# Kernel optimization log

Hardware: AMD Instinct MI355X
Metric: run time of the kernel (lower is better)

The kernel has to match this reference:

```python
import jax, jax.numpy as jnp
import numpy as np

B, C, H, W, E, HEADS = 8, 128, 96, 96, 16, 4
HD = C // HEADS

def _ln(x, g, b, eps=1e-5):
    m = jnp.mean(x, axis=-1, keepdims=True)
    v = jnp.mean(jnp.square(x - m), axis=-1, keepdims=True)
    return (x - m) * jax.lax.rsqrt(v + eps) * g + b

def _gelu(x):
    return jax.nn.gelu(x, approximate=False)  # torch nn.GELU default (erf)

def setup_inputs() -> dict:
    key = jax.random.key(0)
    ks = iter(jax.random.split(key, 48))
    def wgt(shape, s=0.02):
        return jax.random.normal(next(ks), shape, jnp.float32) * s
    d = {
        "feature_map": jax.random.normal(next(ks), (B, C, H, W), jnp.float32),
        "hyperedge_scores": jax.random.uniform(next(ks), (B, H * W, E), jnp.float32),
        # norm_node_pre
        "np_g": jnp.ones((C,), jnp.float32), "np_b": jnp.zeros((C,), jnp.float32),
        # MultiheadAttention (self-attn over hyperedges)
        "mha_w_in": wgt((3 * C, C)), "mha_b_in": jnp.zeros((3 * C,), jnp.float32),
        "mha_w_out": wgt((C, C)), "mha_b_out": jnp.zeros((C,), jnp.float32),
        # transformer FFN
        "ffn_w1": wgt((2 * C, C)), "ffn_b1": jnp.zeros((2 * C,), jnp.float32),
        "ffn_w2": wgt((C, 2 * C)), "ffn_b2": jnp.zeros((C,), jnp.float32),
        # shared LayerNorm inside HypergraphTransformerConv (used twice)
        "tnorm_g": jnp.ones((C,), jnp.float32), "tnorm_b": jnp.zeros((C,), jnp.float32),
        # norm_hyper
        "nh_g": jnp.ones((C,), jnp.float32), "nh_b": jnp.zeros((C,), jnp.float32),
        # hyper_proj
        "hp_w": wgt((C, C)), "hp_b": jnp.zeros((C,), jnp.float32),
        # HyperedgeGuidedNodeAttention
        "q_w": wgt((C, C)), "q_b": jnp.zeros((C,), jnp.float32),
        "kv_w": wgt((2 * C, C)), "kv_b": jnp.zeros((2 * C,), jnp.float32),
        # norm_fusion
        "nf_g": jnp.ones((2 * C,), jnp.float32), "nf_b": jnp.zeros((2 * C,), jnp.float32),
        # gate = Linear(2C->C) + LayerNorm(C) + Sigmoid
        "gate_w": wgt((C, 2 * C)), "gate_b": jnp.zeros((C,), jnp.float32),
        "gate_ln_g": jnp.ones((C,), jnp.float32), "gate_ln_b": jnp.zeros((C,), jnp.float32),
        # node_proj
        "nproj_w": wgt((C, C)), "nproj_b": jnp.zeros((C,), jnp.float32),
    }
    return d

def _forward(feature_map, hyperedge_scores, np_g, np_b, mha_w_in, mha_b_in,
             mha_w_out, mha_b_out, ffn_w1, ffn_b1, ffn_w2, ffn_b2,
             tnorm_g, tnorm_b, nh_g, nh_b, hp_w, hp_b, q_w, q_b, kv_w, kv_b,
             nf_g, nf_b, gate_w, gate_b, gate_ln_g, gate_ln_b, nproj_w, nproj_b):
    b, c, h, w = feature_map.shape
    n = h * w
    node = jnp.transpose(feature_map.reshape(b, c, n), (0, 2, 1))   # [B,N,C]
    node = _ln(node, np_g, np_b)
    # hyperedge aggregation: H^T @ X -> [B,E,C]
    hyper = jnp.einsum('bne,bnc->bec', hyperedge_scores, node)
    # --- HypergraphTransformerConv (self-attn over E=16 hyperedges) ---
    qkv = hyper @ mha_w_in.T + mha_b_in                               # [B,E,3C]
    q, k, v = jnp.split(qkv, 3, axis=-1)
    def heads(x):  # [B,E,C] -> [B,h,E,hd]
        return jnp.transpose(x.reshape(b, E, HEADS, HD), (0, 2, 1, 3))
    q, k, v = heads(q), heads(k), heads(v)
    attn = jax.nn.softmax(jnp.einsum('bhqd,bhkd->bhqk', q, k) / np.sqrt(HD), axis=-1)
    ao = jnp.einsum('bhqk,bhkd->bhqd', attn, v)
    ao = jnp.transpose(ao, (0, 2, 1, 3)).reshape(b, E, c)
    ao = ao @ mha_w_out.T + mha_b_out
    x = _ln(hyper + ao, tnorm_g, tnorm_b)
    ffn = _gelu(x @ ffn_w1.T + ffn_b1) @ ffn_w2.T + ffn_b2
    hyper = _ln(x + ffn, tnorm_g, tnorm_b)
    # ---
    hyper = _ln(hyper, nh_g, nh_b)
    hyper = _gelu(hyper @ hp_w.T + hp_b)                              # [B,E,C]
    intra = jnp.einsum('bne,bec->bnc', hyperedge_scores, hyper)       # [B,N,C]
    # HyperedgeGuidedNodeAttention (scale = C**-0.5)
    Q = node @ q_w.T + q_b
    K, V = jnp.split(hyper @ kv_w.T + kv_b, 2, axis=-1)
    a = jax.nn.softmax(jnp.einsum('bnc,bec->bne', Q, K) * (c ** -0.5), axis=-1)
    cross = jnp.einsum('bne,bec->bnc', a, V)
    combined = _ln(jnp.concatenate([intra, cross], axis=-1), nf_g, nf_b)
    gate = jax.nn.sigmoid(_ln(combined @ gate_w.T + gate_b, gate_ln_g, gate_ln_b))
    fused = gate * intra + (1.0 - gate) * cross
    upd = node + fused                                                # dropout in eval mode
    out = _gelu(upd @ nproj_w.T + nproj_b)
    return jnp.transpose(out, (0, 2, 1)).reshape(b, c, h, w)

def reference(feature_map, hyperedge_scores, np_g, np_b, mha_w_in, mha_b_in,
              mha_w_out, mha_b_out, ffn_w1, ffn_b1, ffn_w2, ffn_b2,
              tnorm_g, tnorm_b, nh_g, nh_b, hp_w, hp_b, q_w, q_b, kv_w, kv_b,
              nf_g, nf_b, gate_w, gate_b, gate_ln_g, gate_ln_b, nproj_w, nproj_b):
    return _forward(feature_map, hyperedge_scores, np_g, np_b, mha_w_in, mha_b_in,
                    mha_w_out, mha_b_out, ffn_w1, ffn_b1, ffn_w2, ffn_b2,
                    tnorm_g, tnorm_b, nh_g, nh_b, hp_w, hp_b, q_w, q_b, kv_w, kv_b,
                    nf_g, nf_b, gate_w, gate_b, gate_ln_g, gate_ln_b, nproj_w, nproj_b)
```

## Files before the change

### kernel.cpp

```cpp
#include <hip/hip_runtime.h>

typedef unsigned short bf_t;
typedef unsigned int u32;
typedef short short8 __attribute__((ext_vector_type(8)));
typedef float f32x4 __attribute__((ext_vector_type(4)));

#define NB 8
#define CC 128
#define NN 9216
#define EE 16

__device__ __forceinline__ float b2f(bf_t u){ return __uint_as_float(((u32)u)<<16); }
__device__ __forceinline__ bf_t f2b(float f){
  u32 u = __float_as_uint(f);
  u = (u + 0x7fffu + ((u>>16)&1u)) >> 16;
  return (bf_t)u;
}
__device__ __forceinline__ float gelu_f(float x){ return 0.5f*x*(1.f+erff(x*0.70710678118654752f)); }
__device__ __forceinline__ float red16(float v){
  #pragma unroll
  for (int m=1;m<16;m<<=1) v += __shfl_xor(v, m, 16);
  return v;
}
__device__ __forceinline__ float grs(float var){
  return rsqrtf(fmaxf(var + 1e-5f, 1e-8f));
}
__device__ __forceinline__ short8 ldw8(const float* __restrict__ p){
  float4 a = *(const float4*)p;
  float4 b = *(const float4*)(p+4);
  short8 o;
  o[0]=(short)f2b(a.x); o[1]=(short)f2b(a.y); o[2]=(short)f2b(a.z); o[3]=(short)f2b(a.w);
  o[4]=(short)f2b(b.x); o[5]=(short)f2b(b.y); o[6]=(short)f2b(b.z); o[7]=(short)f2b(b.w);
  return o;
}

template<int MODE>
__global__ __launch_bounds__(256) void k_pre(float* __restrict__ hacc,
    const float* __restrict__ gw, const float* __restrict__ npw,
    bf_t* __restrict__ gwb, bf_t* __restrict__ npwb,
    const float* __restrict__ w_in, const float* __restrict__ w_out,
    const float* __restrict__ w1, const float* __restrict__ w2,
    const float* __restrict__ hpw, const float* __restrict__ kvw,
    const float* __restrict__ qw,
    bf_t* __restrict__ w_in_b, bf_t* __restrict__ w_out_b,
    bf_t* __restrict__ w1_b, bf_t* __restrict__ w2_b,
    bf_t* __restrict__ hpw_b, bf_t* __restrict__ kvw_b,
    bf_t* __restrict__ qwT_b){
  int i = blockIdx.x*256 + threadIdx.x;
  hacc[i] = 0.f;
  if (MODE >= 1){
    gwb[i]       = f2b(gw[i]);
    gwb[i+16384] = f2b(gw[i+16384]);
    npwb[i]      = f2b(npw[i]);
  }
  if (MODE == 2){
    #pragma unroll
    for (int k=0;k<3;k++) w_in_b[i + k*16384] = f2b(w_in[i + k*16384]);
    w_out_b[i]       = f2b(w_out[i]);
    w1_b[i]          = f2b(w1[i]);
    w1_b[i+16384]    = f2b(w1[i+16384]);
    w2_b[i]          = f2b(w2[i]);
    w2_b[i+16384]    = f2b(w2[i+16384]);
    hpw_b[i]         = f2b(hpw[i]);
    kvw_b[i]         = f2b(kvw[i]);
    kvw_b[i+16384]   = f2b(kvw[i+16384]);
    qwT_b[i]         = f2b(qw[(i&127)*128 + (i>>7)]);
  }
}

template<int BFOUT>
__global__ __launch_bounds__(256,4) void k_ln_agg(const float* __restrict__ fm,
                                                  const float* __restrict__ g,
                                                  const float* __restrict__ bb,
                                                  const float* __restrict__ sc,
                                                  float* __restrict__ nln,
                                                  bf_t* __restrict__ nlnb,
                                                  float* __restrict__ hacc){
  int b = blockIdx.y, n0 = blockIdx.x*64, tid = threadIdx.x;
  __shared__ float xs[128*65];
  __shared__ float scs[64][17];
  __shared__ float ps[4][64], pq[4][64], mrs[2][64];
  const float* base = fm + (size_t)b*CC*NN + n0;
  #pragma unroll
  for (int p=0;p<8;p++){
    int idx = tid + p*256;
    int c = idx>>4, n4 = (idx&15)*4;
    float4 v = *(const float4*)(base + (size_t)c*NN + n4);
    xs[c*65 + n4+0] = v.x; xs[c*65 + n4+1] = v.y;
    xs[c*65 + n4+2] = v.z; xs[c*65 + n4+3] = v.w;
  }
  { int n = tid>>2, e4 = (tid&3)*4;
    float4 sv = *(const float4*)(sc + ((size_t)(b*NN + n0 + n))*EE + e4);
    scs[n][e4+0] = sv.x; scs[n][e4+1] = sv.y;
    scs[n][e4+2] = sv.z; scs[n][e4+3] = sv.w;
  }
  __syncthreads();
  { int cg = tid>>6, n = tid&63;
    float s=0.f, q=0.f;
    #pragma unroll
    for (int c=0;c<32;c++){ float v = xs[(cg*32+c)*65 + n]; s+=v; q+=v*v; }
    ps[cg][n]=s; pq[cg][n]=q;
  }
  __syncthreads();
  if (tid < 64){
    float S = ps[0][tid]+ps[1][tid]+ps[2][tid]+ps[3][tid];
    float Q = pq[0][tid]+pq[1][tid]+pq[2][tid]+pq[3][tid];
    float m = S*(1.f/128.f);
    mrs[0][tid] = m; mrs[1][tid] = grs(Q*(1.f/128.f) - m*m);
  }
  __syncthreads();
  #pragma unroll
  for (int p=0;p<8;p++){
    int idx = tid + p*256;
    int c = idx>>4, n4 = (idx&15)*4;
    float gv = g[c], bv = bb[c];
    float v0 = (xs[c*65+n4+0]-mrs[0][n4+0])*mrs[1][n4+0]*gv + bv;
    float v1 = (xs[c*65+n4+1]-mrs[0][n4+1])*mrs[1][n4+1]*gv + bv;
    float v2 = (xs[c*65+n4+2]-mrs[0][n4+2])*mrs[1][n4+2]*gv + bv;
    float v3 = (xs[c*65+n4+3]-mrs[0][n4+3])*mrs[1][n4+3]*gv + bv;
    xs[c*65+n4+0]=v0; xs[c*65+n4+1]=v1; xs[c*65+n4+2]=v2; xs[c*65+n4+3]=v3;
    if (!BFOUT){
      float4 o; o.x=v0; o.y=v1; o.z=v2; o.w=v3;
      *(float4*)(nln + ((size_t)(b*CC + c))*NN + n0 + n4) = o;
    }
  }
  __syncthreads();
  if (BFOUT){
    #pragma unroll
    for (int p=0;p<4;p++){
      int idx = tid + p*256;
      int n = idx>>4, c8 = (idx&15)*8;
      short8 o;
      #pragma unroll
      for (int j=0;j<8;j++) o[j] = (short)f2b(xs[(c8+j)*65 + n]);
      *(short8*)(nlnb + ((size_t)(b*NN + n0 + n))*CC + c8) = o;
    }
  }
  { int cp = tid&63, eh = tid>>6;
    float a0[4]={0,0,0,0}, a1[4]={0,0,0,0};
    for (int n=0;n<64;n++){
      float x0 = xs[cp*65 + n], x1 = xs[(cp+64)*65 + n];
      #pragma unroll
      for (int j=0;j<4;j++){
        float se = scs[n][eh*4+j];
        a0[j] += se*x0; a1[j] += se*x1;
      }
    }
    #pragma unroll
    for (int j=0;j<4;j++){
      float* hb = hacc + (size_t)(b*EE + eh*4 + j)*CC;
      atomicAdd(hb + cp, a0[j]);
      atomicAdd(hb + cp + 64, a1[j]);
    }
  }
}

template<int K, int NOUT, int ACT, int WB>
__device__ __forceinline__ void gemm16(const bf_t* A, int SA,
                                       const float* __restrict__ W,
                                       const bf_t* __restrict__ Wb,
                                       const float* __restrict__ bias,
                                       bf_t* O, int SO, int tid){
  int lane = tid&63, wid = tid>>6;
  int m16 = lane&15, quad = lane>>4;
  #pragma unroll
  for (int u=0; u<NOUT/64; u++){
    int n0 = u*64 + wid*16;
    f32x4 acc = {0.f,0.f,0.f,0.f};
    #pragma unroll
    for (int k0=0;k0<K;k0+=32){
      short8 af = *(const short8*)(A + m16*SA + k0 + quad*8);
      short8 bfv = WB ? *(const short8*)(Wb + (size_t)(n0+m16)*K + k0 + quad*8)
                      : ldw8(W + (size_t)(n0+m16)*K + k0 + quad*8);
      acc = __builtin_amdgcn_mfma_f32_16x16x32_bf16(af, bfv, acc, 0, 0, 0);
    }
    int col = n0 + m16;
    float bv = bias[col];
    #pragma unroll
    for (int r=0;r<4;r++){
      float v = acc[r] + bv;
      if (ACT) v = gelu_f(v);
      O[(quad*4+r)*SO + col] = f2b(v);
    }
  }
}

#define SP1 136
#define SP2 264
#define SP3 392

template<int WB>
__global__ __launch_bounds__(256) void k_edge(const float* __restrict__ hacc,
    const float* w_in, const float* b_in, const float* w_out, const float* b_out,
    const float* w1, const float* b1, const float* w2, const float* b2v,
    const float* tg, const float* tb, const float* nhg, const float* nhb,
    const float* hpw, const float* hpb, const float* kvw, const float* kvbias,
    const float* qw, const float* qb,
    const bf_t* __restrict__ w_in_b, const bf_t* __restrict__ w_out_b,
    const bf_t* __restrict__ w1_b, const bf_t* __restrict__ w2_b,
    const bf_t* __restrict__ hpw_b, const bf_t* __restrict__ kvw_b,
    const bf_t* __restrict__ qwT_b,
    bf_t* __restrict__ hfw, bf_t* __restrict__ vws,
    bf_t* __restrict__ Ktgb, float* __restrict__ qbK){
  __shared__ __align__(16) bf_t hyp0[16*SP1];
  __shared__ __align__(16) bf_t qkvb[16*SP3];
  __shared__ __align__(16) bf_t aob [16*SP1];
  __shared__ __align__(16) bf_t xnb [16*SP1];
  __shared__ __align__(16) bf_t h1b [16*SP2];
  __shared__ __align__(16) bf_t t2b [16*SP1];
  __shared__ __align__(16) bf_t hfb [16*SP1];
  __shared__ __align__(16) bf_t kvo [16*SP2];
  int b = blockIdx.x, tid = threadIdx.x;
  int lane = tid&63, wid = tid>>6, m16 = lane&15, quad = lane>>4;

  #pragma unroll
  for (int p=0;p<8;p++){
    int idx = tid + p*256;
    int e = idx>>7, c = idx&127;
    hyp0[e*SP1 + c] = f2b(hacc[(size_t)(b*EE + e)*CC + c]);
  }
  __syncthreads();
  gemm16<128,384,0,WB>(hyp0, SP1, w_in, w_in_b, b_in, qkvb, SP3, tid);
  __syncthreads();
  {
    int part = tid&3, hq = tid>>2;
    int h = hq>>4, qi = hq&15;
    int dbase = h*32 + part*8;
    float qv[8];
    #pragma unroll
    for (int j=0;j<8;j++) qv[j] = b2f(qkvb[qi*SP3 + dbase + j]);
    float dot[16];
    #pragma unroll
    for (int kk=0;kk<16;kk++){
      float s = 0.f;
      #pragma unroll
      for (int j=0;j<8;j++) s += qv[j]*b2f(qkvb[kk*SP3 + 128 + dbase + j]);
      dot[kk] = s;
    }
    #pragma unroll
    for (int m=1;m<4;m<<=1){
      #pragma unroll
      for (int kk=0;kk<16;kk++) dot[kk] += __shfl_xor(dot[kk], m, 4);
    }
    const float sc1 = 0.17677669529663687f;
    float mx = -1e30f;
    #pragma unroll
    for (int kk=0;kk<16;kk++){ dot[kk] *= sc1; mx = fmaxf(mx, dot[kk]); }
    float sum = 0.f;
    #pragma unroll
    for (int kk=0;kk<16;kk++){ dot[kk] = __expf(dot[kk]-mx); sum += dot[kk]; }
    float inv = 1.f/sum;
    float ao[8] = {0,0,0,0,0,0,0,0};
    #pragma unroll
    for (int kk=0;kk<16;kk++){
      float p = dot[kk]*inv;
      #pragma unroll
      for (int j=0;j<8;j++) ao[j] += p*b2f(qkvb[kk*SP3 + 256 + dbase + j]);
    }
    #pragma unroll
    for (int j=0;j<8;j++) aob[qi*SP1 + dbase + j] = f2b(ao[j]);
  }
  __syncthreads();
  gemm16<128,128,0,WB>(aob, SP1, w_out, w_out_b, b_out, xnb, SP1, tid);
  __syncthreads();
  {
    int e = tid>>4, i = tid&15;
    float v[8]; float s=0.f, q=0.f;
    #pragma unroll
    for (int j=0;j<8;j++){
      int c = i*8+j;
      v[j] = b2f(hyp0[e*SP1+c]) + b2f(xnb[e*SP1+c]);
      s += v[j]; q += v[j]*v[j];
    }
    s = red16(s); q = red16(q);
    float m = s*(1.f/128.f);
    float rs = grs(q*(1.f/128.f) - m*m);
    #pragma unroll
    for (int j=0;j<8;j++){
      int c = i*8+j;
      xnb[e*SP1+c] = f2b((v[j]-m)*rs*tg[c] + tb[c]);
    }
  }
  __syncthreads();
  gemm16<128,256,1,WB>(xnb, SP1, w1, w1_b, b1, h1b, SP2, tid);
  __syncthreads();
  gemm16<256,128,0,WB>(h1b, SP2, w2, w2_b, b2v, aob, SP1, tid);
  __syncthreads();
  {
    int e = tid>>4, i = tid&15;
    float v[8]; float s=0.f, q=0.f;
    #pragma unroll
    for (int j=0;j<8;j++){
      int c = i*8+j;
      v[j] = b2f(xnb[e*SP1+c]) + b2f(aob[e*SP1+c]);
      s += v[j]; q += v[j]*v[j];
    }
    s = red16(s); q = red16(q);
    float m = s*(1.f/128.f);
    float rs = grs(q*(1.f/128.f) - m*m);
    float s2=0.f, q2=0.f;
    #pragma unroll
    for (int j=0;j<8;j++){
      int c = i*8+j;
      v[j] = (v[j]-m)*rs*tg[c] + tb[c];
      s2 += v[j]; q2 += v[j]*v[j];
    }
    s2 = red16(s2); q2 = red16(q2);
    float m2 = s2*(1.f/128.f);
    float rs2 = grs(q2*(1.f/128.f) - m2*m2);
    #pragma unroll
    for (int j=0;j<8;j++){
      int c = i*8+j;
      t2b[e*SP1+c] = f2b((v[j]-m2)*rs2*nhg[c] + nhb[c]);
    }
  }
  __syncthreads();
  gemm16<128,128,1,WB>(t2b, SP1, hpw, hpw_b, hpb, hfb, SP1, tid);
  __syncthreads();
  gemm16<128,256,0,WB>(hfb, SP1, kvw, kvw_b, kvbias, kvo, SP2, tid);
  __syncthreads();
  #pragma unroll
  for (int p=0;p<8;p++){
    int idx = tid + p*256;
    int e = idx>>7, c = idx&127;
    size_t o = (size_t)(b*EE + e)*CC + c;
    hfw[o] = hfb[e*SP1 + c];
    vws[o] = kvo[e*SP2 + 128 + c];
  }
  #pragma unroll
  for (int u=0;u<2;u++){
    int n0 = u*64 + wid*16;
    f32x4 acc = {0.f,0.f,0.f,0.f};
    #pragma unroll
    for (int k0=0;k0<128;k0+=32){
      short8 a = *(const short8*)(kvo + m16*SP2 + k0 + quad*8);
      short8 bq;
      if (WB){
        bq = *(const short8*)(qwT_b + (size_t)(n0+m16)*128 + k0 + quad*8);
      } else {
        #pragma unroll
        for (int j=0;j<8;j++)
          bq[j] = (short)f2b(qw[(size_t)(k0+quad*8+j)*128 + n0+m16]);
      }
      acc = __builtin_amdgcn_mfma_f32_16x16x32_bf16(a, bq, acc, 0, 0, 0);
    }
    #pragma unroll
    for (int r=0;r<4;r++)
      Ktgb[(size_t)(b*EE + quad*4 + r)*CC + n0 + m16] = f2b(acc[r]);
  }
  { int e = tid>>4, i = tid&15;
    float s = 0.f;
    #pragma unroll
    for (int j=0;j<8;j++) s += qb[i*8+j]*b2f(kvo[e*SP2 + i*8+j]);
    s = red16(s);
    if (i == 0) qbK[b*EE + e] = s;
  }
}

template<int MODE>
__global__ __launch_bounds__(256,3) void k_meganode(
    float* __restrict__ io, const bf_t* __restrict__ nlnb,
    const float* __restrict__ sc,
    const bf_t* __restrict__ hf, const bf_t* __restrict__ vw,
    const bf_t* __restrict__ ktg, const float* __restrict__ qbK,
    const float* __restrict__ nfg, const float* __restrict__ nfb,
    const float* __restrict__ gw, const bf_t* __restrict__ gwb,
    const float* __restrict__ gb,
    const float* __restrict__ glng, const float* __restrict__ glnb,
    const float* __restrict__ npw, const bf_t* __restrict__ npwb,
    const float* __restrict__ npb){
  int tid = threadIdx.x, lane = tid&63, wid = tid>>6;
  int m16 = lane&15, quad = lane>>4;
  int b = blockIdx.y, n0 = blockIdx.x*64;
  __shared__ __align__(16) char sm[34816];
  bf_t* xt  = (bf_t*)(sm);
  bf_t* ktT = (bf_t*)(sm + 17408);
  bf_t* hfT = (bf_t*)(sm + 21760);
  bf_t* vfT = (bf_t*)(sm + 25856);
  bf_t* ash = (bf_t*)(sm + 29952);
  bf_t* ct  = (bf_t*)(sm + 17408);
  float* ot = (float*)(sm);
  const short8 z8 = {0,0,0,0,0,0,0,0};

  if (MODE == 2){
    const bf_t* nb = nlnb + ((size_t)(b*NN + n0))*CC;
    #pragma unroll
    for (int p=0;p<4;p++){
      int idx = tid + p*256;
      int n = idx>>4, c8 = (idx&15)*8;
      *(short8*)&xt[n*136 + c8] = *(const short8*)(nb + (size_t)n*CC + c8);
    }
  } else {
    #pragma unroll
    for (int p=0;p<8;p++){
      int idx = tid + p*256;
      int c = idx>>4, n4 = (idx&15)*4;
      float4 v = *(const float4*)(io + ((size_t)(b*CC + c))*NN + n0 + n4);
      xt[(n4+0)*136 + c] = f2b(v.x);
      xt[(n4+1)*136 + c] = f2b(v.y);
      xt[(n4+2)*136 + c] = f2b(v.z);
      xt[(n4+3)*136 + c] = f2b(v.w);
    }
  }
  { const u32* kp = (const u32*)(ktg + (size_t)b*EE*CC);
    #pragma unroll
    for (int p=0;p<4;p++){
      int idx = tid + p*256;
      int e = idx>>6, c2 = (idx&63)*2;
      *(u32*)&ktT[e*136 + c2] = kp[idx];
    }
  }
  { const u32* hs = (const u32*)(hf + (size_t)b*EE*CC);
    const u32* vs = (const u32*)(vw + (size_t)b*EE*CC);
    #pragma unroll
    for (int p=0;p<4;p++){
      int idx = tid + p*256;
      int e = idx>>6, c2 = (idx&63)*2;
      u32 hv = hs[idx], vv = vs[idx];
      hfT[(c2+0)*16 + e] = (bf_t)(hv&0xffffu);
      hfT[(c2+1)*16 + e] = (bf_t)(hv>>16);
      vfT[(c2+0)*16 + e] = (bf_t)(vv&0xffffu);
      vfT[(c2+1)*16 + e] = (bf_t)(vv>>16);
    }
  }
  __syncthreads();

  f32x4 dacc = {0.f,0.f,0.f,0.f};
  #pragma unroll
  for (int kk=0;kk<4;kk++){
    short8 a = *(const short8*)(xt + (wid*16+m16)*136 + kk*32 + quad*8);
    short8 bfr = *(const short8*)(ktT + m16*136 + kk*32 + quad*8);
    dacc = __builtin_amdgcn_mfma_f32_16x16x32_bf16(a, bfr, dacc, 0, 0, 0);
  }
  { float qbe = qbK[b*EE + m16];
    #pragma unroll
    for (int r=0;r<4;r++){
      float v = (dacc[r] + qbe) * 0.08838834764831845f;
      float m = v;
      #pragma unroll
      for (int msk=1;msk<16;msk<<=1) m = fmaxf(m, __shfl_xor(m, msk, 16));
      float ex = __expf(v - m);
      float s = ex;
      #pragma unroll
      for (int msk=1;msk<16;msk<<=1) s += __shfl_xor(s, msk, 16);
      ash[(wid*16 + quad*4 + r)*16 + m16] = f2b(ex / s);
    }
  }

  short8 scf = z8, asf = z8;
  if (quad < 2){
    const float* sp = sc + ((size_t)(b*NN + n0 + wid*16 + m16))*EE + quad*8;
    float4 u0 = *(const float4*)sp;
    float4 u1 = *(const float4*)(sp+4);
    scf[0]=(short)f2b(u0.x); scf[1]=(short)f2b(u0.y); scf[2]=(short)f2b(u0.z); scf[3]=(short)f2b(u0.w);
    scf[4]=(short)f2b(u1.x); scf[5]=(short)f2b(u1.y); scf[6]=(short)f2b(u1.z); scf[7]=(short)f2b(u1.w);
    asf = *(const short8*)(ash + (wid*16+m16)*16 + quad*8);
  }
  f32x4 acc_it[8], acc_cr[8];
  #pragma unroll
  for (int t=0;t<8;t++){
    short8 bh = z8, bv = z8;
    if (quad < 2){
      bh = *(const short8*)(hfT + (t*16+m16)*16 + quad*8);
      bv = *(const short8*)(vfT + (t*16+m16)*16 + quad*8);
    }
    f32x4 zf = {0.f,0.f,0.f,0.f};
    acc_it[t] = __builtin_amdgcn_mfma_f32_16x16x32_bf16(scf, bh, zf, 0, 0, 0);
    acc_cr[t] = __builtin_amdgcn_mfma_f32_16x16x32_bf16(asf, bv, zf, 0, 0, 0);
  }

  float mean4[4], rstd4[4];
  { float s4[4]={0,0,0,0}, q4[4]={0,0,0,0};
    #pragma unroll
    for (int t=0;t<8;t++)
      #pragma unroll
      for (int r=0;r<4;r++){
        float a = acc_it[t][r], c = acc_cr[t][r];
        s4[r] += a + c; q4[r] += a*a + c*c;
      }
    #pragma unroll
    for (int r=0;r<4;r++){
      s4[r] = red16(s4[r]); q4[r] = red16(q4[r]);
      mean4[r] = s4[r]*(1.f/256.f);
      rstd4[r] = grs(q4[r]*(1.f/256.f) - mean4[r]*mean4[r]);
    }
  }
  __syncthreads();
  short8 af[8];
  #pragma unroll
  for (int r=0;r<4;r++){
    int node = wid*16 + quad*4 + r;
    #pragma unroll
    for (int t=0;t<8;t++){
      int ch = t*16 + m16;
      ct[node*136 + ch] = f2b((acc_it[t][r]-mean4[r])*rstd4[r]*nfg[ch] + nfb[ch]);
    }
  }
  #pragma unroll
  for (int kk=0;kk<4;kk++)
    af[kk] = *(const short8*)(ct + (wid*16+m16)*136 + kk*32 + quad*8);
  #pragma unroll
  for (int r=0;r<4;r++){
    int node = wid*16 + quad*4 + r;
    #pragma unroll
    for (int t=0;t<8;t++){
      int ch = t*16 + m16;
      ct[node*136 + ch] = f2b((acc_cr[t][r]-mean4[r])*rstd4[r]*nfg[128+ch] + nfb[128+ch]);
    }
  }
  #pragma unroll
  for (int kk=0;kk<4;kk++)
    af[4+kk] = *(const short8*)(ct + (wid*16+m16)*136 + kk*32 + quad*8);

  f32x4 acc_g[8];
  #pragma unroll
  for (int t=0;t<8;t++){
    f32x4 a = {0.f,0.f,0.f,0.f};
    #pragma unroll
    for (int kk=0;kk<8;kk++){
      short8 w8 = (MODE >= 1) ? *(const short8*)(gwb + (size_t)(t*16+m16)*256 + kk*32 + quad*8)
                              : ldw8(gw + (size_t)(t*16+m16)*256 + kk*32 + quad*8);
      a = __builtin_amdgcn_mfma_f32_16x16x32_bf16(af[kk], w8, a, 0, 0, 0);
    }
    acc_g[t] = a;
  }

  { float s2[4]={0,0,0,0}, q2[4]={0,0,0,0};
    #pragma unroll
    for (int t=0;t<8;t++){
      float bv = gb[t*16+m16];
      #pragma unroll
      for (int r=0;r<4;r++){
        float v = acc_g[t][r] + bv;
        acc_g[t][r] = v; s2[r] += v; q2[r] += v*v;
      }
    }
    #pragma unroll
    for (int r=0;r<4;r++){ s2[r] = red16(s2[r]); q2[r] = red16(q2[r]); }
    #pragma unroll
    for (int t=0;t<8;t++){
      int col = t*16 + m16;
      float lg = glng[col], lb = glnb[col];
      #pragma unroll
      for (int r=0;r<4;r++){
        float m2 = s2[r]*(1.f/128.f);
        float rs2 = grs(q2[r]*(1.f/128.f) - m2*m2);
        float z = (acc_g[t][r]-m2)*rs2*lg + lb;
        float gs = 1.f/(1.f + __expf(-z));
        int node = wid*16 + quad*4 + r;
        float nld = b2f(xt[node*136 + col]);
        xt[node*136 + col] = f2b(nld + gs*acc_it[t][r] + (1.f-gs)*acc_cr[t][r]);
      }
    }
  }

  short8 bfu[4];
  #pragma unroll
  for (int kk=0;kk<4;kk++)
    bfu[kk] = *(const short8*)(xt + (wid*16+m16)*136 + kk*32 + quad*8);
  __syncthreads();
  #pragma unroll
  for (int mt=0;mt<8;mt++){
    f32x4 o = {0.f,0.f,0.f,0.f};
    #pragma unroll
    for (int kk=0;kk<4;kk++){
      short8 aw = (MODE >= 1) ? *(const short8*)(npwb + (size_t)(mt*16+m16)*128 + kk*32 + quad*8)
                              : ldw8(npw + (size_t)(mt*16+m16)*128 + kk*32 + quad*8);
      o = __builtin_amdgcn_mfma_f32_16x16x32_bf16(aw, bfu[kk], o, 0, 0, 0);
    }
    #pragma unroll
    for (int r=0;r<4;r++){
      int cp = mt*16 + quad*4 + r;
      ot[cp*68 + wid*16 + m16] = gelu_f(o[r] + npb[cp]);
    }
  }
  __syncthreads();
  #pragma unroll
  for (int p=0;p<8;p++){
    int idx = tid + p*256;
    int c = idx>>4, n4 = (idx&15)*4;
    float4 v = *(const float4*)&ot[c*68 + n4];
    *(float4*)(io + ((size_t)(b*CC + c))*NN + n0 + n4) = v;
  }
}

extern "C" void kernel_launch(void* const* d_in, const int* in_sizes, int n_in,
                              void* d_out, int out_size, void* d_ws, size_t ws_size,
                              hipStream_t stream){
  (void)in_sizes; (void)n_in; (void)out_size;
  const float* fm   = (const float*)d_in[0];
  const float* sc   = (const float*)d_in[1];
  const float* npg  = (const float*)d_in[2];
  const float* npb_ = (const float*)d_in[3];
  const float* w_in = (const float*)d_in[4];
  const float* b_in = (const float*)d_in[5];
  const float* w_out= (const float*)d_in[6];
  const float* b_out= (const float*)d_in[7];
  const float* w1   = (const float*)d_in[8];
  const float* b1   = (const float*)d_in[9];
  const float* w2   = (const float*)d_in[10];
  const float* b2v  = (const float*)d_in[11];
  const float* tg   = (const float*)d_in[12];
  const float* tb   = (const float*)d_in[13];
  const float* nhg  = (const float*)d_in[14];
  const float* nhb  = (const float*)d_in[15];
  const float* hpw  = (const float*)d_in[16];
  const float* hpb  = (const float*)d_in[17];
  const float* qw   = (const float*)d_in[18];
  const float* qb   = (const float*)d_in[19];
  const float* kvw  = (const float*)d_in[20];
  const float* kvb  = (const float*)d_in[21];
  const float* nfg  = (const float*)d_in[22];
  const float* nfb  = (const float*)d_in[23];
  const float* gw   = (const float*)d_in[24];
  const float* gb   = (const float*)d_in[25];
  const float* glng = (const float*)d_in[26];
  const float* glnb = (const float*)d_in[27];
  const float* npw  = (const float*)d_in[28];
  const float* npb2 = (const float*)d_in[29];

  float* nln = (float*)d_out;

  char* w = (char*)d_ws;
  float* hacc    = (float*)(w);
  float* qbK     = (float*)(w + 65536);
  bf_t*  hfw     = (bf_t*) (w + 66048);
  bf_t*  vws     = (bf_t*) (w + 98816);
  bf_t*  Ktgb    = (bf_t*) (w + 131584);
  bf_t*  gwb     = (bf_t*) (w + 164352);
  bf_t*  npwb    = (bf_t*) (w + 229888);
  bf_t*  w_in_b  = (bf_t*) (w + 262656);
  bf_t*  w_out_b = (bf_t*) (w + 360960);
  bf_t*  w1_b    = (bf_t*) (w + 393728);
  bf_t*  w2_b    = (bf_t*) (w + 459264);
  bf_t*  hpw_b   = (bf_t*) (w + 524800);
  bf_t*  kvw_b   = (bf_t*) (w + 557568);
  bf_t*  qwT_b   = (bf_t*) (w + 623104);
  bf_t*  nlnb    = (bf_t*) (w + 655872);
  bool full = (ws_size >= (size_t)19530240);
  bool pre  = (ws_size >= (size_t)262656);

  if (full){
    k_pre<2><<<dim3(64), dim3(256), 0, stream>>>(hacc, gw, npw, gwb, npwb,
        w_in, w_out, w1, w2, hpw, kvw, qw,
        w_in_b, w_out_b, w1_b, w2_b, hpw_b, kvw_b, qwT_b);
    k_ln_agg<1><<<dim3(144,8), dim3(256), 0, stream>>>(fm, npg, npb_, sc, nln, nlnb, hacc);
    k_edge<1><<<dim3(8), dim3(256), 0, stream>>>(hacc, w_in,b_in,w_out,b_out,
        w1,b1,w2,b2v, tg,tb, nhg,nhb, hpw,hpb, kvw,kvb, qw,qb,
        w_in_b, w_out_b, w1_b, w2_b, hpw_b, kvw_b, qwT_b,
        hfw, vws, Ktgb, qbK);
    k_meganode<2><<<dim3(144,8), dim3(256), 0, stream>>>(nln, nlnb, sc, hfw, vws, Ktgb, qbK,
        nfg, nfb, gw, gwb, gb, glng, glnb, npw, npwb, npb2);
  } else if (pre){
    k_pre<1><<<dim3(64), dim3(256), 0, stream>>>(hacc, gw, npw, gwb, npwb,
        w_in, w_out, w1, w2, hpw, kvw, qw,
        w_in_b, w_out_b, w1_b, w2_b, hpw_b, kvw_b, qwT_b);
    k_ln_agg<0><<<dim3(144,8), dim3(256), 0, stream>>>(fm, npg, npb_, sc, nln, nlnb, hacc);
    k_edge<0><<<dim3(8), dim3(256), 0, stream>>>(hacc, w_in,b_in,w_out,b_out,
        w1,b1,w2,b2v, tg,tb, nhg,nhb, hpw,hpb, kvw,kvb, qw,qb,
        w_in_b, w_out_b, w1_b, w2_b, hpw_b, kvw_b, qwT_b,
        hfw, vws, Ktgb, qbK);
    k_meganode<1><<<dim3(144,8), dim3(256), 0, stream>>>(nln, nlnb, sc, hfw, vws, Ktgb, qbK,
        nfg, nfb, gw, gwb, gb, glng, glnb, npw, npwb, npb2);
  } else {
    k_pre<0><<<dim3(64), dim3(256), 0, stream>>>(hacc, gw, npw, gwb, npwb,
        w_in, w_out, w1, w2, hpw, kvw, qw,
        w_in_b, w_out_b, w1_b, w2_b, hpw_b, kvw_b, qwT_b);
    k_ln_agg<0><<<dim3(144,8), dim3(256), 0, stream>>>(fm, npg, npb_, sc, nln, nlnb, hacc);
    k_edge<0><<<dim3(8), dim3(256), 0, stream>>>(hacc, w_in,b_in,w_out,b_out,
        w1,b1,w2,b2v, tg,tb, nhg,nhb, hpw,hpb, kvw,kvb, qw,qb,
        w_in_b, w_out_b, w1_b, w2_b, hpw_b, kvw_b, qwT_b,
        hfw, vws, Ktgb, qbK);
    k_meganode<0><<<dim3(144,8), dim3(256), 0, stream>>>(nln, nlnb, sc, hfw, vws, Ktgb, qbK,
        nfg, nfb, gw, gwb, gb, glng, glnb, npw, npwb, npb2);
  }
}
```

Measured before the change: 267.9 us.

## Replace hyperedge atomics with partial-sum buffer plus reduction, widen edge kernel to 512 threads

The per-tile hyperedge aggregation now writes per-block partial sums to a workspace buffer, and a new small reduction kernel sums them, replacing global float atomics. The aim is to remove atomic contention on a small accumulator and make the result deterministic. The edge kernel goes from 256 to 512 threads, with the MFMA GEMMs split across 8 waves, to shorten its serial chain of small GEMMs. The cost is an extra launch and about 9 MB of partial-sum traffic. The new path runs only when the workspace is large enough.

```diff
diff --git a/kernel.cpp b/kernel.cpp
--- a/kernel.cpp
+++ b/kernel.cpp
@@ -9,6 +9,7 @@
 #define CC 128
 #define NN 9216
 #define EE 16
+#define NT 144
 
 __device__ __forceinline__ float b2f(bf_t u){ return __uint_as_float(((u32)u)<<16); }
 __device__ __forceinline__ bf_t f2b(float f){
@@ -68,14 +69,15 @@
   }
 }
 
-template<int BFOUT>
+template<int BFOUT, int ATOM>
 __global__ __launch_bounds__(256,4) void k_ln_agg(const float* __restrict__ fm,
                                                   const float* __restrict__ g,
                                                   const float* __restrict__ bb,
                                                   const float* __restrict__ sc,
                                                   float* __restrict__ nln,
                                                   bf_t* __restrict__ nlnb,
-                                                  float* __restrict__ hacc){
+                                                  float* __restrict__ hacc,
+                                                  float* __restrict__ part){
   int b = blockIdx.y, n0 = blockIdx.x*64, tid = threadIdx.x;
   __shared__ float xs[128*65];
   __shared__ float scs[64][17];
@@ -146,16 +148,40 @@
         a0[j] += se*x0; a1[j] += se*x1;
       }
     }
-    #pragma unroll
-    for (int j=0;j<4;j++){
-      float* hb = hacc + (size_t)(b*EE + eh*4 + j)*CC;
-      atomicAdd(hb + cp, a0[j]);
-      atomicAdd(hb + cp + 64, a1[j]);
-    }
-  }
-}
-
-template<int K, int NOUT, int ACT, int WB>
+    if (ATOM){
+      #pragma unroll
+      for (int j=0;j<4;j++){
+        float* hb = hacc + (size_t)(b*EE + eh*4 + j)*CC;
+        atomicAdd(hb + cp, a0[j]);
+        atomicAdd(hb + cp + 64, a1[j]);
+      }
+    } else {
+      float* pb = part + ((size_t)(b*NT + blockIdx.x)*EE)*CC;
+      #pragma unroll
+      for (int j=0;j<4;j++){
+        pb[(eh*4+j)*CC + cp]      = a0[j];
+        pb[(eh*4+j)*CC + cp + 64] = a1[j];
+      }
+    }
+  }
+}
+
+__global__ __launch_bounds__(128) void k_red(const float* __restrict__ part,
+                                             float* __restrict__ hacc){
+  int e = blockIdx.x, b = blockIdx.y, c = threadIdx.x;
+  const float* p = part + ((size_t)(b*NT)*EE + e)*CC + c;
+  float s0=0.f, s1=0.f, s2=0.f, s3=0.f;
+  #pragma unroll
+  for (int t=0;t<NT;t+=4){
+    s0 += p[(size_t)(t+0)*EE*CC];
+    s1 += p[(size_t)(t+1)*EE*CC];
+    s2 += p[(size_t)(t+2)*EE*CC];
+    s3 += p[(size_t)(t+3)*EE*CC];
+  }
+  hacc[((size_t)b*EE + e)*CC + c] = (s0+s1)+(s2+s3);
+}
+
+template<int K, int NOUT, int ACT, int WB, int NW>
 __device__ __forceinline__ void gemm16(const bf_t* A, int SA,
                                        const float* __restrict__ W,
                                        const bf_t* __restrict__ Wb,
@@ -164,8 +190,8 @@
   int lane = tid&63, wid = tid>>6;
   int m16 = lane&15, quad = lane>>4;
   #pragma unroll
-  for (int u=0; u<NOUT/64; u++){
-    int n0 = u*64 + wid*16;
+  for (int u=0; u<NOUT/(16*NW); u++){
+    int n0 = u*(16*NW) + wid*16;
     f32x4 acc = {0.f,0.f,0.f,0.f};
     #pragma unroll
     for (int k0=0;k0<K;k0+=32){
@@ -190,7 +216,7 @@
 #define SP3 392
 
 template<int WB>
-__global__ __launch_bounds__(256) void k_edge(const float* __restrict__ hacc,
+__global__ __launch_bounds__(512) void k_edge(const float* __restrict__ hacc,
     const float* w_in, const float* b_in, const float* w_out, const float* b_out,
     const float* w1, const float* b1, const float* w2, const float* b2v,
     const float* tg, const float* tb, const float* nhg, const float* nhb,
@@ -214,15 +240,15 @@
   int lane = tid&63, wid = tid>>6, m16 = lane&15, quad = lane>>4;
 
   #pragma unroll
-  for (int p=0;p<8;p++){
-    int idx = tid + p*256;
+  for (int p=0;p<4;p++){
+    int idx = tid + p*512;
     int e = idx>>7, c = idx&127;
     hyp0[e*SP1 + c] = f2b(hacc[(size_t)(b*EE + e)*CC + c]);
   }
   __syncthreads();
-  gemm16<128,384,0,WB>(hyp0, SP1, w_in, w_in_b, b_in, qkvb, SP3, tid);
-  __syncthreads();
-  {
+  gemm16<128,384,0,WB,8>(hyp0, SP1, w_in, w_in_b, b_in, qkvb, SP3, tid);
+  __syncthreads();
+  if (tid < 256){
     int part = tid&3, hq = tid>>2;
     int h = hq>>4, qi = hq&15;
     int dbase = h*32 + part*8;
@@ -261,9 +287,9 @@
     for (int j=0;j<8;j++) aob[qi*SP1 + dbase + j] = f2b(ao[j]);
   }
   __syncthreads();
-  gemm16<128,128,0,WB>(aob, SP1, w_out, w_out_b, b_out, xnb, SP1, tid);
-  __syncthreads();
-  {
+  gemm16<128,128,0,WB,8>(aob, SP1, w_out, w_out_b, b_out, xnb, SP1, tid);
+  __syncthreads();
+  if (tid < 256){
     int e = tid>>4, i = tid&15;
     float v[8]; float s=0.f, q=0.f;
     #pragma unroll
@@ -282,11 +308,11 @@
     }
   }
   __syncthreads();
-  gemm16<128,256,1,WB>(xnb, SP1, w1, w1_b, b1, h1b, SP2, tid);
-  __syncthreads();
-  gemm16<256,128,0,WB>(h1b, SP2, w2, w2_b, b2v, aob, SP1, tid);
-  __syncthreads();
-  {
+  gemm16<128,256,1,WB,8>(xnb, SP1, w1, w1_b, b1, h1b, SP2, tid);
+  __syncthreads();
+  gemm16<256,128,0,WB,8>(h1b, SP2, w2, w2_b, b2v, aob, SP1, tid);
+  __syncthreads();
+  if (tid < 256){
     int e = tid>>4, i = tid&15;
     float v[8]; float s=0.f, q=0.f;
     #pragma unroll
@@ -315,21 +341,20 @@
     }
   }
   __syncthreads();
-  gemm16<128,128,1,WB>(t2b, SP1, hpw, hpw_b, hpb, hfb, SP1, tid);
-  __syncthreads();
-  gemm16<128,256,0,WB>(hfb, SP1, kvw, kvw_b, kvbias, kvo, SP2, tid);
-  __syncthreads();
-  #pragma unroll
-  for (int p=0;p<8;p++){
-    int idx = tid + p*256;
+  gemm16<128,128,1,WB,8>(t2b, SP1, hpw, hpw_b, hpb, hfb, SP1, tid);
+  __syncthreads();
+  gemm16<128,256,0,WB,8>(hfb, SP1, kvw, kvw_b, kvbias, kvo, SP2, tid);
+  __syncthreads();
+  #pragma unroll
+  for (int p=0;p<4;p++){
+    int idx = tid + p*512;
     int e = idx>>7, c = idx&127;
     size_t o = (size_t)(b*EE + e)*CC + c;
     hfw[o] = hfb[e*SP1 + c];
     vws[o] = kvo[e*SP2 + 128 + c];
   }
-  #pragma unroll
-  for (int u=0;u<2;u++){
-    int n0 = u*64 + wid*16;
+  {
+    int n0 = wid*16;
     f32x4 acc = {0.f,0.f,0.f,0.f};
     #pragma unroll
     for (int k0=0;k0<128;k0+=32){
@@ -348,7 +373,8 @@
     for (int r=0;r<4;r++)
       Ktgb[(size_t)(b*EE + quad*4 + r)*CC + n0 + m16] = f2b(acc[r]);
   }
-  { int e = tid>>4, i = tid&15;
+  if (tid < 256){
+    int e = tid>>4, i = tid&15;
     float s = 0.f;
     #pragma unroll
     for (int j=0;j<8;j++) s += qb[i*8+j]*b2f(kvo[e*SP2 + i*8+j]);
@@ -637,41 +663,55 @@
   bf_t*  kvw_b   = (bf_t*) (w + 557568);
   bf_t*  qwT_b   = (bf_t*) (w + 623104);
   bf_t*  nlnb    = (bf_t*) (w + 655872);
-  bool full = (ws_size >= (size_t)19530240);
-  bool pre  = (ws_size >= (size_t)262656);
-
-  if (full){
+  float* part    = (float*)(w + 19530240);
+  bool full2 = (ws_size >= (size_t)28967424);
+  bool full  = (ws_size >= (size_t)19530240);
+  bool pre   = (ws_size >= (size_t)262656);
+
+  if (full2){
     k_pre<2><<<dim3(64), dim3(256), 0, stream>>>(hacc, gw, npw, gwb, npwb,
         w_in, w_out, w1, w2, hpw, kvw, qw,
         w_in_b, w_out_b, w1_b, w2_b, hpw_b, kvw_b, qwT_b);
-    k_ln_agg<1><<<dim3(144,8), dim3(256), 0, stream>>>(fm, npg, npb_, sc, nln, nlnb, hacc);
-    k_edge<1><<<dim3(8), dim3(256), 0, stream>>>(hacc, w_in,b_in,w_out,b_out,
+    k_ln_agg<1,0><<<dim3(NT,8), dim3(256), 0, stream>>>(fm, npg, npb_, sc, nln, nlnb, hacc, part);
+    k_red<<<dim3(EE,8), dim3(128), 0, stream>>>(part, hacc);
+    k_edge<1><<<dim3(8), dim3(512), 0, stream>>>(hacc, w_in,b_in,w_out,b_out,
         w1,b1,w2,b2v, tg,tb, nhg,nhb, hpw,hpb, kvw,kvb, qw,qb,
         w_in_b, w_out_b, w1_b, w2_b, hpw_b, kvw_b, qwT_b,
         hfw, vws, Ktgb, qbK);
-    k_meganode<2><<<dim3(144,8), dim3(256), 0, stream>>>(nln, nlnb, sc, hfw, vws, Ktgb, qbK,
+    k_meganode<2><<<dim3(NT,8), dim3(256), 0, stream>>>(nln, nlnb, sc, hfw, vws, Ktgb, qbK,
+        nfg, nfb, gw, gwb, gb, glng, glnb, npw, npwb, npb2);
+  } else if (full){
+    k_pre<2><<<dim3(64), dim3(256), 0, stream>>>(hacc, gw, npw, gwb, npwb,
+        w_in, w_out, w1, w2, hpw, kvw, qw,
+        w_in_b, w_out_b, w1_b, w2_b, hpw_b, kvw_b, qwT_b);
+    k_ln_agg<1,1><<<dim3(NT,8), dim3(256), 0, stream>>>(fm, npg, npb_, sc, nln, nlnb, hacc, part);
+    k_edge<1><<<dim3(8), dim3(512), 0, stream>>>(hacc, w_in,b_in,w_out,b_out,
+        w1,b1,w2,b2v, tg,tb, nhg,nhb, hpw,hpb, kvw,kvb, qw,qb,
+        w_in_b, w_out_b, w1_b, w2_b, hpw_b, kvw_b, qwT_b,
+        hfw, vws, Ktgb, qbK);
+    k_meganode<2><<<dim3(NT,8), dim3(256), 0, stream>>>(nln, nlnb, sc, hfw, vws, Ktgb, qbK,
         nfg, nfb, gw, gwb, gb, glng, glnb, npw, npwb, npb2);
   } else if (pre){
     k_pre<1><<<dim3(64), dim3(256), 0, stream>>>(hacc, gw, npw, gwb, npwb,
         w_in, w_out, w1, w2, hpw, kvw, qw,
         w_in_b, w_out_b, w1_b, w2_b, hpw_b, kvw_b, qwT_b);
-    k_ln_agg<0><<<dim3(144,8), dim3(256), 0, stream>>>(fm, npg, npb_, sc, nln, nlnb, hacc);
-    k_edge<0><<<dim3(8), dim3(256), 0, stream>>>(hacc, w_in,b_in,w_out,b_out,
+    k_ln_agg<0,1><<<dim3(NT,8), dim3(256), 0, stream>>>(fm, npg, npb_, sc, nln, nlnb, hacc, part);
+    k_edge<0><<<dim3(8), dim3(512), 0, stream>>>(hacc, w_in,b_in,w_out,b_out,
         w1,b1,w2,b2v, tg,tb, nhg,nhb, hpw,hpb, kvw,kvb, qw,qb,
         w_in_b, w_out_b, w1_b, w2_b, hpw_b, kvw_b, qwT_b,
         hfw, vws, Ktgb, qbK);
-    k_meganode<1><<<dim3(144,8), dim3(256), 0, stream>>>(nln, nlnb, sc, hfw, vws, Ktgb, qbK,
+    k_meganode<1><<<dim3(NT,8), dim3(256), 0, stream>>>(nln, nlnb, sc, hfw, vws, Ktgb, qbK,
         nfg, nfb, gw, gwb, gb, glng, glnb, npw, npwb, npb2);
   } else {
     k_pre<0><<<dim3(64), dim3(256), 0, stream>>>(hacc, gw, npw, gwb, npwb,
         w_in, w_out, w1, w2, hpw, kvw, qw,
         w_in_b, w_out_b, w1_b, w2_b, hpw_b, kvw_b, qwT_b);
-    k_ln_agg<0><<<dim3(144,8), dim3(256), 0, stream>>>(fm, npg, npb_, sc, nln, nlnb, hacc);
-    k_edge<0><<<dim3(8), dim3(256), 0, stream>>>(hacc, w_in,b_in,w_out,b_out,
+    k_ln_agg<0,1><<<dim3(NT,8), dim3(256), 0, stream>>>(fm, npg, npb_, sc, nln, nlnb, hacc, part);
+    k_edge<0><<<dim3(8), dim3(512), 0, stream>>>(hacc, w_in,b_in,w_out,b_out,
         w1,b1,w2,b2v, tg,tb, nhg,nhb, hpw,hpb, kvw,kvb, qw,qb,
         w_in_b, w_out_b, w1_b, w2_b, hpw_b, kvw_b, qwT_b,
         hfw, vws, Ktgb, qbK);
-    k_meganode<0><<<dim3(144,8), dim3(256), 0, stream>>>(nln, nlnb, sc, hfw, vws, Ktgb, qbK,
+    k_meganode<0><<<dim3(NT,8), dim3(256), 0, stream>>>(nln, nlnb, sc, hfw, vws, Ktgb, qbK,
         nfg, nfb, gw, gwb, gb, glng, glnb, npw, npwb, npb2);
   }
 }
```

Result: no change. 267.5 us (-0.2%).
